# Kernel optimization log

Hardware: AMD Instinct MI355X
Metric: run time of the kernel (lower is better)

The kernel has to match this reference:

```python
import jax, jax.numpy as jnp
import numpy as np

B, L, D, H = 2, 2048, 1024, 16
HD = D // H
ROPE_BASE = 10000.0


def _chain_info(lengths):
    """lengths: [B, L] int, chain lengths packed at the front, zeros after.
    Returns per-position within-chain positions (RoPE resets per chain),
    chain ids, and a validity mask."""
    def one(row):
        csum = jnp.cumsum(row)                      # [L]
        total = csum[-1]
        p = jnp.arange(L)
        cid = jnp.searchsorted(csum, p, side='right')  # chain id per position
        prev = jnp.where(cid > 0, csum[jnp.clip(cid - 1, 0, L - 1)], 0)
        valid = p < total
        pos = jnp.where(valid, p - prev, 0).astype(jnp.float32)
        return pos, cid, valid
    return jax.vmap(one)(lengths)


def _rope_tables(pos):
    # pos: [B, L] float -> cos/sin [B, L, 1, HD]
    inv_freq = 1.0 / (ROPE_BASE ** (jnp.arange(0, HD, 2, dtype=jnp.float32) / HD))
    freqs = pos[..., None] * inv_freq               # [B, L, HD/2]
    emb = jnp.concatenate([freqs, freqs], axis=-1)  # [B, L, HD]
    return jnp.cos(emb)[:, :, None, :], jnp.sin(emb)[:, :, None, :]


def _apply_rope(x, cos, sin):
    d = x.shape[-1]
    x1, x2 = x[..., : d // 2], x[..., d // 2:]
    return x * cos + jnp.concatenate([-x2, x1], axis=-1) * sin


def _branch(x, Wqkv, bqkv, cos, sin, allowed):
    # x: [B, L, D]; allowed: [B, L, L] bool attention mask for this branch
    qkv = x @ Wqkv.T + bqkv                          # [B, L, 3D]
    qkv = qkv.reshape(B, L, 3, H, HD)
    q, k, v = qkv[:, :, 0], qkv[:, :, 1], qkv[:, :, 2]
    q = q * (HD ** -0.5)
    q = _apply_rope(q, cos, sin)
    k = _apply_rope(k, cos, sin)
    scores = jnp.einsum('bthd,bshd->bhts', q, k)     # [B, H, L, L]
    scores = jnp.where(allowed[:, None], scores, -jnp.inf)
    probs = jax.nn.softmax(scores, axis=-1)
    probs = jnp.where(jnp.isnan(probs), 0.0, probs)  # fully-masked rows -> 0
    out = jnp.einsum('bhts,bshd->bthd', probs, v)    # [B, L, H, HD]
    return out.reshape(B, L, D)


def setup_inputs() -> dict:
    key = jax.random.key(0)
    ks = jax.random.split(key, 7)
    s = 0.02
    lens = np.zeros((B, L), np.int64)
    lens[0, :8] = [300, 250, 200, 400, 350, 248, 150, 100]   # sum 1998
    lens[1, :6] = [512, 400, 300, 360, 276, 200]             # sum 2048
    return {
        'hidden_states': jax.random.normal(ks[0], (B, L, D), jnp.float32),
        'attention_mask_in_length': jnp.asarray(lens),
        'Wqkv_intra': jax.random.normal(ks[1], (3 * D, D), jnp.float32) * s,
        'bqkv_intra': jnp.zeros((3 * D,), jnp.float32),
        'Wqkv_inter': jax.random.normal(ks[2], (3 * D, D), jnp.float32) * s,
        'bqkv_inter': jnp.zeros((3 * D,), jnp.float32),
        'Wout': jax.random.normal(ks[3], (D, D), jnp.float32) * s,
        'bout': jnp.zeros((D,), jnp.float32),
    }


def reference(hidden_states, attention_mask_in_length, Wqkv_intra, bqkv_intra,
              Wqkv_inter, bqkv_inter, Wout, bout):
    pos, cid, valid = _chain_info(attention_mask_in_length)
    cos, sin = _rope_tables(pos)
    same_chain = cid[:, :, None] == cid[:, None, :]          # [B, L, L]
    key_valid = valid[:, None, :]                            # [B, 1, L]
    allowed_intra = same_chain & key_valid
    allowed_inter = (~same_chain) & key_valid
    out_intra = _branch(hidden_states, Wqkv_intra, bqkv_intra, cos, sin, allowed_intra)
    out_inter = _branch(hidden_states, Wqkv_inter, bqkv_inter, cos, sin, allowed_inter)
    return (out_intra + out_inter) @ Wout.T + bout
```

## Files before the change

kernel.cpp:

```cpp
#include <hip/hip_runtime.h>
#include <hip/hip_bf16.h>
#include <stdint.h>

#define B 2
#define L 2048
#define D 1024
#define H 16
#define HD 64
#define NT (L / 64)
#define INVALID_CID 0x40000000
#define BHLHD ((size_t)B * H * L * HD)

typedef __hip_bfloat16 bf16;
typedef __attribute__((ext_vector_type(8))) short short8;
typedef __attribute__((ext_vector_type(4))) float floatx4;
typedef __attribute__((ext_vector_type(4))) unsigned int uint4v;

static __device__ __forceinline__ short f2bf(float f) {
    bf16 h = __float2bfloat16(f);
    return *reinterpret_cast<short*>(&h);
}

static __device__ __forceinline__ void async_copy16(const void* g, void* l) {
    __builtin_amdgcn_global_load_lds((__attribute__((address_space(1))) void*)g,
                                     (__attribute__((address_space(3))) void*)l,
                                     16, 0, 0);
}

__global__ void chain_kernel(const int* __restrict__ lens,
                             float* __restrict__ pos, int* __restrict__ cid,
                             int4* __restrict__ tinfo)
{
    __shared__ int csum[L];
    __shared__ int cids[L];
    __shared__ int part[256];
    int b = blockIdx.x;
    int t = threadIdx.x;

    int loc[8];
    int s = 0;
    #pragma unroll
    for (int j = 0; j < 8; ++j) { s += lens[b * L + t * 8 + j]; loc[j] = s; }
    part[t] = s;
    __syncthreads();
    if (t == 0) {
        int acc = 0;
        for (int i = 0; i < 256; ++i) { int v = part[i]; part[i] = acc; acc += v; }
    }
    __syncthreads();
    int base = part[t];
    #pragma unroll
    for (int j = 0; j < 8; ++j) csum[t * 8 + j] = base + loc[j];
    __syncthreads();

    int total = csum[L - 1];
    for (int p = t; p < L; p += 256) {
        int cv;
        if (p < total) {
            int lo = 0, hi = L;
            while (lo < hi) {
                int mid = (lo + hi) >> 1;
                if (csum[mid] <= p) lo = mid + 1; else hi = mid;
            }
            int prev = (lo > 0) ? csum[lo - 1] : 0;
            pos[b * L + p] = (float)(p - prev);
            cv = lo;
        } else {
            pos[b * L + p] = 0.f;
            cv = INVALID_CID;
        }
        cids[p] = cv;
        cid[b * L + p] = cv;
    }
    __syncthreads();
    if (t < NT) {
        int mn = 0x7fffffff, mx = -1, any = 0, all = 1;
        for (int j = 0; j < 64; ++j) {
            int cv = cids[t * 64 + j];
            if (cv != INVALID_CID) { any = 1; mn = min(mn, cv); mx = max(mx, cv); }
            else all = 0;
        }
        tinfo[b * NT + t] = make_int4(mn, mx, any | (all << 1), 0);
    }
}

__global__ void rope_table(const float* __restrict__ pos, float2* __restrict__ tab)
{
    int idx = blockIdx.x * 256 + threadIdx.x;
    int j = idx & 31, l = idx >> 5;
    float invf = exp2f(-(float)j * (13.287712379549449f / 32.f));
    float ang = pos[l] * invf;
    tab[idx] = make_float2(cosf(ang), sinf(ang));
}

__global__ void cast_all(const float* __restrict__ x,  const float* __restrict__ Wi,
                         const float* __restrict__ We, const float* __restrict__ Wo,
                         bf16* __restrict__ xb, bf16* __restrict__ Wib,
                         bf16* __restrict__ Web, bf16* __restrict__ Wob)
{
    int bid = blockIdx.x;
    const float* src; bf16* dst; int base;
    if      (bid < 4096)  { src = x;  dst = xb;  base = bid; }
    else if (bid < 7168)  { src = Wi; dst = Wib; base = bid - 4096; }
    else if (bid < 10240) { src = We; dst = Web; base = bid - 7168; }
    else                  { src = Wo; dst = Wob; base = bid - 10240; }
    int i = (base * 256 + threadIdx.x) * 4;
    float4 v = *(const float4*)(src + i);
    dst[i + 0] = __float2bfloat16(v.x);
    dst[i + 1] = __float2bfloat16(v.y);
    dst[i + 2] = __float2bfloat16(v.z);
    dst[i + 3] = __float2bfloat16(v.w);
}

__global__ __launch_bounds__(256, 4) void gemm_qkv(
    const bf16* __restrict__ A, const bf16* __restrict__ Bw,
    const float* __restrict__ bi, const float* __restrict__ be,
    const float2* __restrict__ tab,
    bf16* __restrict__ Qo, bf16* __restrict__ Ko, bf16* __restrict__ Vto)
{
    __shared__ short Smem[2 * 128 * 32];
    short* As = Smem;
    short* Bs = Smem + 128 * 32;

    int tid = threadIdx.x;
    int wave = tid >> 6, lane = tid & 63;
    int i15 = lane & 15, q8 = lane >> 4;
    int wm = wave & 1, wn = wave >> 1;
    int m0 = blockIdx.y * 128, n0 = blockIdx.x * 128;
    const int K = D;

    floatx4 acc[4][4];
    #pragma unroll
    for (int mt = 0; mt < 4; ++mt)
        #pragma unroll
        for (int nt = 0; nt < 4; ++nt) acc[mt][nt] = (floatx4){0.f, 0.f, 0.f, 0.f};

    const short* gA = (const short*)A  + (size_t)(m0 + wave * 32 + (lane >> 2)) * K + (lane & 3) * 8;
    const short* gB = (const short*)Bw + (size_t)(n0 + wave * 32 + (lane >> 2)) * K + (lane & 3) * 8;
    short* lA = As + wave * 1024;
    short* lB = Bs + wave * 1024;

    for (int kt = 0; kt < K; kt += 32) {
        __syncthreads();
        async_copy16(gA + kt,          lA);
        async_copy16(gA + 16 * K + kt, lA + 512);
        async_copy16(gB + kt,          lB);
        async_copy16(gB + 16 * K + kt, lB + 512);
        __syncthreads();

        short8 af[4], bfr[4];
        #pragma unroll
        for (int mt = 0; mt < 4; ++mt)
            af[mt] = *(const short8*)&As[(wm * 64 + mt * 16 + i15) * 32 + q8 * 8];
        #pragma unroll
        for (int nt = 0; nt < 4; ++nt)
            bfr[nt] = *(const short8*)&Bs[(wn * 64 + nt * 16 + i15) * 32 + q8 * 8];
        #pragma unroll
        for (int mt = 0; mt < 4; ++mt)
            #pragma unroll
            for (int nt = 0; nt < 4; ++nt)
                acc[mt][nt] = __builtin_amdgcn_mfma_f32_16x16x32_bf16(af[mt], bfr[nt], acc[mt][nt], 0, 0, 0);
    }

    int nb = n0 + wn * 64;
    int segw = nb >> 10;
    int br = (segw >= 3);
    int st = segw - 3 * br;
    int h = (nb >> 6) & (H - 1);
    int b = m0 >> 11;
    int lb = (m0 & (L - 1)) + wm * 64;

    float bv[4];
    #pragma unroll
    for (int nt = 0; nt < 4; ++nt) {
        int n = nb + nt * 16 + i15;
        bv[nt] = (n < 3 * D) ? bi[n] : be[n - 3 * D];
    }

    if (st != 2) {
        bf16* out = (st == 0 ? Qo : Ko) + (size_t)br * BHLHD;
        const size_t bh = (size_t)(b * H + h) * L;
        float qs = (st == 0) ? 0.18033688011111772f : 1.0f;
        #pragma unroll
        for (int mt = 0; mt < 4; ++mt) {
            #pragma unroll
            for (int rg = 0; rg < 4; ++rg) {
                int m = m0 + wm * 64 + mt * 16 + q8 * 4 + rg;
                int l = lb + mt * 16 + q8 * 4 + rg;
                float2 cs0 = tab[(size_t)m * 32 + i15];
                float2 cs1 = tab[(size_t)m * 32 + 16 + i15];
                size_t orow = (bh + l) * HD;
                #pragma unroll
                for (int nt = 0; nt < 4; ++nt) {
                    float x  = acc[mt][nt][rg] + bv[nt];
                    float pr = acc[mt][nt ^ 2][rg] + bv[nt ^ 2];
                    float cc = (nt & 1) ? cs1.x : cs0.x;
                    float ss = (nt & 1) ? cs1.y : cs0.y;
                    float v = qs * (x * cc + ((nt < 2) ? -pr : pr) * ss);
                    out[orow + nt * 16 + i15] = __float2bfloat16(v);
                }
            }
        }
    } else {
        bf16* out = Vto + (size_t)br * BHLHD;
        const size_t bhd = (size_t)(b * H + h) * HD;
        __syncthreads();
        short* vts = Smem + wave * 64 * 20;
        #pragma unroll
        for (int mt = 0; mt < 4; ++mt) {
            #pragma unroll
            for (int nt = 0; nt < 4; ++nt) {
                uint2 w;
                w.x = (unsigned)(unsigned short)f2bf(acc[mt][nt][0] + bv[nt]) |
                      ((unsigned)(unsigned short)f2bf(acc[mt][nt][1] + bv[nt]) << 16);
                w.y = (unsigned)(unsigned short)f2bf(acc[mt][nt][2] + bv[nt]) |
                      ((unsigned)(unsigned short)f2bf(acc[mt][nt][3] + bv[nt]) << 16);
                *(uint2*)&vts[(nt * 16 + i15) * 20 + q8 * 4] = w;
            }
            uint2 r0 = *(const uint2*)&vts[lane * 20 + 0];
            uint2 r1 = *(const uint2*)&vts[lane * 20 + 4];
            uint2 r2 = *(const uint2*)&vts[lane * 20 + 8];
            uint2 r3 = *(const uint2*)&vts[lane * 20 + 12];
            size_t ga = (bhd + lane) * L + lb + mt * 16;
            uint4v v0 = (uint4v){r0.x, r0.y, r1.x, r1.y};
            uint4v v1 = (uint4v){r2.x, r2.y, r3.x, r3.y};
            *(uint4v*)&out[ga]     = v0;
            *(uint4v*)&out[ga + 8] = v1;
        }
    }
}

__global__ __launch_bounds__(256, 4) void gemm128(
    const bf16* __restrict__ A, const bf16* __restrict__ Bw,
    const float* __restrict__ bias, void* __restrict__ Cout,
    int M, int N, int K, int c_bf16)
{
    __shared__ short As[128 * 32];
    __shared__ short Bs[128 * 32];

    int tid = threadIdx.x;
    int wave = tid >> 6, lane = tid & 63;
    int i15 = lane & 15, q8 = lane >> 4;
    int wm = wave & 1, wn = wave >> 1;
    int m0 = blockIdx.y * 128, n0 = blockIdx.x * 128;

    floatx4 acc[4][4];
    #pragma unroll
    for (int mt = 0; mt < 4; ++mt)
        #pragma unroll
        for (int nt = 0; nt < 4; ++nt) acc[mt][nt] = (floatx4){0.f, 0.f, 0.f, 0.f};

    const short* gA = (const short*)A  + (size_t)(m0 + wave * 32 + (lane >> 2)) * K + (lane & 3) * 8;
    const short* gB = (const short*)Bw + (size_t)(n0 + wave * 32 + (lane >> 2)) * K + (lane & 3) * 8;
    short* lA = As + wave * 1024;
    short* lB = Bs + wave * 1024;

    for (int kt = 0; kt < K; kt += 32) {
        __syncthreads();
        async_copy16(gA + kt,          lA);
        async_copy16(gA + 16 * K + kt, lA + 512);
        async_copy16(gB + kt,          lB);
        async_copy16(gB + 16 * K + kt, lB + 512);
        __syncthreads();

        short8 af[4], bfr[4];
        #pragma unroll
        for (int mt = 0; mt < 4; ++mt)
            af[mt] = *(const short8*)&As[(wm * 64 + mt * 16 + i15) * 32 + q8 * 8];
        #pragma unroll
        for (int nt = 0; nt < 4; ++nt)
            bfr[nt] = *(const short8*)&Bs[(wn * 64 + nt * 16 + i15) * 32 + q8 * 8];
        #pragma unroll
        for (int mt = 0; mt < 4; ++mt)
            #pragma unroll
            for (int nt = 0; nt < 4; ++nt)
                acc[mt][nt] = __builtin_amdgcn_mfma_f32_16x16x32_bf16(af[mt], bfr[nt], acc[mt][nt], 0, 0, 0);
    }

    #pragma unroll
    for (int nt = 0; nt < 4; ++nt) {
        int n = n0 + wn * 64 + nt * 16 + i15;
        float bv = bias[n];
        #pragma unroll
        for (int mt = 0; mt < 4; ++mt) {
            #pragma unroll
            for (int rg = 0; rg < 4; ++rg) {
                int m = m0 + wm * 64 + mt * 16 + q8 * 4 + rg;
                float v = acc[mt][nt][rg] + bv;
                if (c_bf16) ((bf16*)Cout)[(size_t)m * N + n] = __float2bfloat16(v);
                else        ((float*)Cout)[(size_t)m * N + n] = v;
            }
        }
    }
}

__global__ __launch_bounds__(256, 4) void attn9(
    const bf16* __restrict__ Qg, const bf16* __restrict__ Kgg, const bf16* __restrict__ Vtgg,
    const int* __restrict__ cid, const int4* __restrict__ tinfo,
    bf16* __restrict__ Out)
{
    __shared__ short Ks[2][64][72];
    __shared__ short Vs[2][64][72];
    __shared__ int cls0_s[NT], cls1_s[NT];
    __shared__ int list_s[2][NT];
    __shared__ int nlist_s[2];

    int tid = threadIdx.x;
    int wave = tid >> 6, lane = tid & 63;
    int i15 = lane & 15, q8 = lane >> 4;
    int workid = ((blockIdx.x & 7) << 7) | (blockIdx.x >> 3);
    int qt = workid & (NT - 1);
    int h  = (workid >> 5) & (H - 1);
    int b  = workid >> 9;
    int q0 = qt * 64;
    const size_t bh  = (size_t)(b * H + h) * L;
    const size_t bhd = (size_t)(b * H + h) * HD;

    int cq = cid[b * L + q0 + wave * 16 + i15];

    int4 qinf = tinfo[b * NT + qt];
    int qall = (qinf.z >> 1) & 1;

    if (tid < NT) {
        int4 ki = tinfo[b * NT + tid];
        int kany = ki.z & 1, kall = (ki.z >> 1) & 1;
        bool disjoint = (ki.x > qinf.y) || (ki.y < qinf.x);
        bool mono = qall && kall && (qinf.x == qinf.y) && (ki.x == ki.y) && (qinf.x == ki.x);
        cls0_s[tid] = (!kany || disjoint) ? 0 : (mono ? 2 : 1);
        cls1_s[tid] = (!kany || mono) ? 0 : ((kall && disjoint) ? 2 : 1);
    }
    __syncthreads();
    if (tid < 2) {
        const int* cls = tid ? cls1_s : cls0_s;
        int n = 0;
        for (int t = 0; t < NT; ++t) {
            int c = cls[t];
            if (c) list_s[tid][n++] = (t * 64) | ((c == 2) << 16);
        }
        nlist_s[tid] = n;
    }
    __syncthreads();

    int r = tid >> 2, ccol = (tid & 3) * 16;
    int sr = ((((r >> 2) & 1) | ((r >> 5) << 1)) << 4) | (((r >> 3) & 3) << 2) | (r & 3);

    floatx4 accO[2][4];
    #pragma unroll
    for (int br = 0; br < 2; ++br)
        #pragma unroll
        for (int t = 0; t < 4; ++t) accO[br][t] = (floatx4){0.f, 0.f, 0.f, 0.f};
    float lsum[2] = {0.f, 0.f};

    #pragma unroll
    for (int br = 0; br < 2; ++br) {
        const short* Qb    = (const short*)Qg   + (size_t)br * BHLHD;
        const short* Kbase = (const short*)Kgg  + (size_t)br * BHLHD + (bh + r) * HD + ccol;
        const short* Vbase = (const short*)Vtgg + (size_t)br * BHLHD + (bhd + r) * L + ccol;
        int n = nlist_s[br];

        short8 qf0, qf1;
        {
            const short* qp = Qb + (bh + q0 + wave * 16 + i15) * HD + q8 * 8;
            qf0 = *(const short8*)(qp);
            qf1 = *(const short8*)(qp + 32);
        }

        int4 pk0, pk1, pv0, pv1;
        int cur = 0;
        if (n > 0) {
            cur = list_s[br][0];
            int kt0 = cur & 0xffff;
            pk0 = *(const int4*)(Kbase + (size_t)kt0 * HD);
            pk1 = *(const int4*)(Kbase + (size_t)kt0 * HD + 8);
            pv0 = *(const int4*)(Vbase + kt0);
            pv1 = *(const int4*)(Vbase + kt0 + 8);
        }
        __syncthreads();

        for (int i = 0; i < n; ++i) {
            int kt = cur & 0xffff, full = cur >> 16;
            int buf = i & 1;

            *(int4*)&Ks[buf][sr][ccol]     = pk0;
            *(int4*)&Ks[buf][sr][ccol + 8] = pk1;
            *(int4*)&Vs[buf][r][ccol]      = pv0;
            *(int4*)&Vs[buf][r][ccol + 8]  = pv1;
            __syncthreads();

            if (i + 1 < n) {
                cur = list_s[br][i + 1];
                int nk = cur & 0xffff;
                pk0 = *(const int4*)(Kbase + (size_t)nk * HD);
                pk1 = *(const int4*)(Kbase + (size_t)nk * HD + 8);
                pv0 = *(const int4*)(Vbase + nk);
                pv1 = *(const int4*)(Vbase + nk + 8);
            }

            unsigned int dl[4], dh[4];
            #pragma unroll
            for (int t = 0; t < 4; ++t) {
                short8 b0 = *(const short8*)&Ks[buf][t * 16 + i15][q8 * 8];
                short8 b1 = *(const short8*)&Ks[buf][t * 16 + i15][32 + q8 * 8];

                floatx4 accS = (floatx4){0.f, 0.f, 0.f, 0.f};
                accS = __builtin_amdgcn_mfma_f32_16x16x32_bf16(b0, qf0, accS, 0, 0, 0);
                accS = __builtin_amdgcn_mfma_f32_16x16x32_bf16(b1, qf1, accS, 0, 0, 0);

                if (!full) {
                    int4 ck4 = *(const int4*)(cid + b * L + kt + (q8 << 3) + ((t & 1) << 2) + ((t >> 1) << 5));
                    int ckr[4] = {ck4.x, ck4.y, ck4.z, ck4.w};
                    #pragma unroll
                    for (int rg = 0; rg < 4; ++rg) {
                        bool kv = (ckr[rg] != INVALID_CID);
                        bool match = (cq == ckr[rg]);
                        bool ok = kv && (br ? !match : match);
                        accS[rg] = ok ? accS[rg] : -1e30f;
                    }
                }

                float p0 = __builtin_amdgcn_exp2f(accS[0]);
                float p1 = __builtin_amdgcn_exp2f(accS[1]);
                float p2 = __builtin_amdgcn_exp2f(accS[2]);
                float p3 = __builtin_amdgcn_exp2f(accS[3]);
                lsum[br] += (p0 + p1) + (p2 + p3);
                dl[t] = (unsigned)(unsigned short)f2bf(p0) | ((unsigned)(unsigned short)f2bf(p1) << 16);
                dh[t] = (unsigned)(unsigned short)f2bf(p2) | ((unsigned)(unsigned short)f2bf(p3) << 16);
            }

            union { uint4v u; short8 s; } pa0, pa1;
            pa0.u = (uint4v){dl[0], dh[0], dl[1], dh[1]};
            pa1.u = (uint4v){dl[2], dh[2], dl[3], dh[3]};

            #pragma unroll
            for (int dt = 0; dt < 4; ++dt) {
                short8 vf0 = *(const short8*)&Vs[buf][dt * 16 + i15][q8 * 8];
                short8 vf1 = *(const short8*)&Vs[buf][dt * 16 + i15][32 + q8 * 8];
                accO[br][dt] = __builtin_amdgcn_mfma_f32_16x16x32_bf16(pa0.s, vf0, accO[br][dt], 0, 0, 0);
                accO[br][dt] = __builtin_amdgcn_mfma_f32_16x16x32_bf16(pa1.s, vf1, accO[br][dt], 0, 0, 0);
            }
        }
    }

    float inv[2][4];
    #pragma unroll
    for (int br = 0; br < 2; ++br) {
        float ls = lsum[br];
        ls += __shfl_xor(ls, 16, 64);
        ls += __shfl_xor(ls, 32, 64);
        #pragma unroll
        for (int rg = 0; rg < 4; ++rg) {
            float lv = __shfl(ls, q8 * 4 + rg, 64);
            inv[br][rg] = (lv > 0.f) ? 1.f / lv : 0.f;
        }
    }

    #pragma unroll
    for (int t = 0; t < 4; ++t)
        #pragma unroll
        for (int rg = 0; rg < 4; ++rg) {
            size_t idx = (size_t)(b * L + q0 + wave * 16 + q8 * 4 + rg) * D + h * HD + t * 16 + i15;
            float o = accO[0][t][rg] * inv[0][rg] + accO[1][t][rg] * inv[1][rg];
            Out[idx] = __float2bfloat16(o);
        }
}

extern "C" void kernel_launch(void* const* d_in, const int* in_sizes, int n_in,
                              void* d_out, int out_size, void* d_ws, size_t ws_size,
                              hipStream_t stream)
{
    const float* x    = (const float*)d_in[0];
    const int*   mlen = (const int*)  d_in[1];
    const float* Wi   = (const float*)d_in[2];
    const float* bi   = (const float*)d_in[3];
    const float* We   = (const float*)d_in[4];
    const float* be   = (const float*)d_in[5];
    const float* Wo   = (const float*)d_in[6];
    const float* bo   = (const float*)d_in[7];

    char* ws = (char*)d_ws;
    size_t off = 0;
    auto alloc = [&](size_t bytes) {
        void* p = ws + off;
        off += (bytes + 255) & ~(size_t)255;
        return p;
    };
    bf16*  x_b   = (bf16*) alloc((size_t)B * L * D * 2);
    bf16*  Wi_b  = (bf16*) alloc((size_t)3 * D * D * 2);
    bf16*  We_b  = (bf16*) alloc((size_t)3 * D * D * 2);
    bf16*  Wo_b  = (bf16*) alloc((size_t)D * D * 2);
    bf16*  q_b   = (bf16*) alloc(2 * BHLHD * 2);
    bf16*  k_b   = (bf16*) alloc(2 * BHLHD * 2);
    bf16*  vt_b  = (bf16*) alloc(2 * BHLHD * 2);
    bf16*  sum_b = (bf16*) alloc((size_t)B * L * D * 2);
    float* pos   = (float*)alloc((size_t)B * L * 4);
    int*   cid   = (int*)  alloc((size_t)B * L * 4);
    int4*  tinfo = (int4*) alloc((size_t)B * NT * 16);
    float2* rtab = (float2*)alloc((size_t)B * L * 32 * 8);
    (void)ws_size; (void)n_in; (void)in_sizes; (void)out_size;

    chain_kernel<<<B, 256, 0, stream>>>(mlen, pos, cid, tinfo);
    rope_table<<<B * L * 32 / 256, 256, 0, stream>>>(pos, rtab);

    cast_all<<<11264, 256, 0, stream>>>(x, Wi, We, Wo, x_b, Wi_b, We_b, Wo_b);

    dim3 gq(6 * D / 128, B * L / 128);
    gemm_qkv<<<gq, 256, 0, stream>>>(x_b, Wi_b, bi, be, rtab, q_b, k_b, vt_b);

    attn9<<<B * H * NT, 256, 0, stream>>>(q_b, k_b, vt_b, cid, tinfo, sum_b);

    dim3 go(D / 128, B * L / 128);
    gemm128<<<go, 256, 0, stream>>>(sum_b, Wo_b, bo, d_out, B * L, D, D, 0);
}
```

Before: 293.2 us.

## Process 128 query rows per attention block with 8 waves sharing K/V tiles

The attention kernel now handles a 128-row query tile per block using 512 threads (8 waves), so each K/V tile staged in shared memory is reused by twice as many queries, and each thread loads half as much per tile. Tile classification merges the two 64-row query tiles' chain info, which can make the skip lists less selective (more masked tiles processed). The grid is halved and occupancy bounds change to 2 blocks of 512.

```diff
diff --git a/kernel.cpp b/kernel.cpp
--- a/kernel.cpp
+++ b/kernel.cpp
@@ -8,6 +8,7 @@
 #define H 16
 #define HD 64
 #define NT (L / 64)
+#define NQT (L / 128)
 #define INVALID_CID 0x40000000
 #define BHLHD ((size_t)B * H * L * HD)
 
@@ -294,7 +295,7 @@
     }
 }
 
-__global__ __launch_bounds__(256, 4) void attn9(
+__global__ __launch_bounds__(512, 2) void attn10(
     const bf16* __restrict__ Qg, const bf16* __restrict__ Kgg, const bf16* __restrict__ Vtgg,
     const int* __restrict__ cid, const int4* __restrict__ tinfo,
     bf16* __restrict__ Out)
@@ -308,17 +309,22 @@
     int tid = threadIdx.x;
     int wave = tid >> 6, lane = tid & 63;
     int i15 = lane & 15, q8 = lane >> 4;
-    int workid = ((blockIdx.x & 7) << 7) | (blockIdx.x >> 3);
-    int qt = workid & (NT - 1);
-    int h  = (workid >> 5) & (H - 1);
-    int b  = workid >> 9;
-    int q0 = qt * 64;
+    int workid = ((blockIdx.x & 7) << 6) | (blockIdx.x >> 3);
+    int qt = workid & (NQT - 1);
+    int h  = (workid >> 4) & (H - 1);
+    int b  = workid >> 8;
+    int q0 = qt * 128;
     const size_t bh  = (size_t)(b * H + h) * L;
     const size_t bhd = (size_t)(b * H + h) * HD;
 
     int cq = cid[b * L + q0 + wave * 16 + i15];
 
-    int4 qinf = tinfo[b * NT + qt];
+    int4 qa = tinfo[b * NT + 2 * qt];
+    int4 qb4 = tinfo[b * NT + 2 * qt + 1];
+    int4 qinf;
+    qinf.x = min(qa.x, qb4.x);
+    qinf.y = max(qa.y, qb4.y);
+    qinf.z = ((qa.z | qb4.z) & 1) | (qa.z & qb4.z & 2);
     int qall = (qinf.z >> 1) & 1;
 
     if (tid < NT) {
@@ -341,7 +347,7 @@
     }
     __syncthreads();
 
-    int r = tid >> 2, ccol = (tid & 3) * 16;
+    int r = tid >> 3, c8 = (tid & 7) * 8;
     int sr = ((((r >> 2) & 1) | ((r >> 5) << 1)) << 4) | (((r >> 3) & 3) << 2) | (r & 3);
 
     floatx4 accO[2][4];
@@ -354,8 +360,8 @@
     #pragma unroll
     for (int br = 0; br < 2; ++br) {
         const short* Qb    = (const short*)Qg   + (size_t)br * BHLHD;
-        const short* Kbase = (const short*)Kgg  + (size_t)br * BHLHD + (bh + r) * HD + ccol;
-        const short* Vbase = (const short*)Vtgg + (size_t)br * BHLHD + (bhd + r) * L + ccol;
+        const short* Kbase = (const short*)Kgg  + (size_t)br * BHLHD + (bh + r) * HD + c8;
+        const short* Vbase = (const short*)Vtgg + (size_t)br * BHLHD + (bhd + r) * L + c8;
         int n = nlist_s[br];
 
         short8 qf0, qf1;
@@ -365,15 +371,13 @@
             qf1 = *(const short8*)(qp + 32);
         }
 
-        int4 pk0, pk1, pv0, pv1;
+        int4 pk, pv;
         int cur = 0;
         if (n > 0) {
             cur = list_s[br][0];
             int kt0 = cur & 0xffff;
-            pk0 = *(const int4*)(Kbase + (size_t)kt0 * HD);
-            pk1 = *(const int4*)(Kbase + (size_t)kt0 * HD + 8);
-            pv0 = *(const int4*)(Vbase + kt0);
-            pv1 = *(const int4*)(Vbase + kt0 + 8);
+            pk = *(const int4*)(Kbase + (size_t)kt0 * HD);
+            pv = *(const int4*)(Vbase + kt0);
         }
         __syncthreads();
 
@@ -381,19 +385,15 @@
             int kt = cur & 0xffff, full = cur >> 16;
             int buf = i & 1;
 
-            *(int4*)&Ks[buf][sr][ccol]     = pk0;
-            *(int4*)&Ks[buf][sr][ccol + 8] = pk1;
-            *(int4*)&Vs[buf][r][ccol]      = pv0;
-            *(int4*)&Vs[buf][r][ccol + 8]  = pv1;
+            *(int4*)&Ks[buf][sr][c8] = pk;
+            *(int4*)&Vs[buf][r][c8]  = pv;
             __syncthreads();
 
             if (i + 1 < n) {
                 cur = list_s[br][i + 1];
                 int nk = cur & 0xffff;
-                pk0 = *(const int4*)(Kbase + (size_t)nk * HD);
-                pk1 = *(const int4*)(Kbase + (size_t)nk * HD + 8);
-                pv0 = *(const int4*)(Vbase + nk);
-                pv1 = *(const int4*)(Vbase + nk + 8);
+                pk = *(const int4*)(Kbase + (size_t)nk * HD);
+                pv = *(const int4*)(Vbase + nk);
             }
 
             unsigned int dl[4], dh[4];
@@ -506,7 +506,7 @@
     dim3 gq(6 * D / 128, B * L / 128);
     gemm_qkv<<<gq, 256, 0, stream>>>(x_b, Wi_b, bi, be, rtab, q_b, k_b, vt_b);
 
-    attn9<<<B * H * NT, 256, 0, stream>>>(q_b, k_b, vt_b, cid, tinfo, sum_b);
+    attn10<<<B * H * NQT, 512, 0, stream>>>(q_b, k_b, vt_b, cid, tinfo, sum_b);
 
     dim3 go(D / 128, B * L / 128);
     gemm128<<<go, 256, 0, stream>>>(sum_b, Wo_b, bo, d_out, B * L, D, D, 0);
```

Result: no change. 288.4 us (-1.6%).
